# Performance work log

Measured on AMD Instinct MI355X. Metric: run time of the kernel, lower is better.

The kernel has to match this reference:

```python
import jax, jax.numpy as jnp
import numpy as np

N = 100000
NNZ = 1600000
C_IN = 128
C_OUT = 128


def setup_inputs() -> dict:
    key = jax.random.key(0)
    ks = jax.random.split(key, 9)
    phi_indices = jax.random.randint(ks[0], (2, NNZ), 0, N, dtype=jnp.int64)
    phi_values = jax.random.uniform(ks[1], (NNZ,), dtype=jnp.float32)
    phi_inverse_indices = jax.random.randint(ks[2], (2, NNZ), 0, N, dtype=jnp.int64)
    phi_inverse_values = jax.random.uniform(ks[3], (NNZ,), dtype=jnp.float32)
    # feature matrix is N x C_IN sparse: row in [0,N), col in [0,C_IN)
    f_rows = jax.random.randint(ks[4], (NNZ,), 0, N, dtype=jnp.int64)
    f_cols = jax.random.randint(ks[5], (NNZ,), 0, C_IN, dtype=jnp.int64)
    feature_indices = jnp.stack([f_rows, f_cols], axis=0)
    feature_values = jax.random.uniform(ks[6], (NNZ,), dtype=jnp.float32)
    # xavier-uniform weight, diagonal filter ~ U(0.9, 1.1)
    limit = float(np.sqrt(6.0 / (C_IN + C_OUT)))
    weight_matrix = jax.random.uniform(ks[7], (C_IN, C_OUT), minval=-limit, maxval=limit, dtype=jnp.float32)
    diagonal_weight_filter = jax.random.uniform(ks[8], (N, 1), minval=0.9, maxval=1.1, dtype=jnp.float32)
    return {
        "phi_indices": phi_indices,
        "phi_values": phi_values,
        "phi_inverse_indices": phi_inverse_indices,
        "phi_inverse_values": phi_inverse_values,
        "feature_indices": feature_indices,
        "feature_values": feature_values,
        "weight_matrix": weight_matrix,
        "diagonal_weight_filter": diagonal_weight_filter,
        "dropout": 0,
    }


def _spmm(indices, values, dense, n_rows):
    # sparse (n_rows x K) @ dense (K x C): gather dense rows by col index,
    # scale by values, scatter-add into output rows.
    rows, cols = indices[0], indices[1]
    contrib = values[:, None] * dense[cols]  # [nnz, C]
    return jax.ops.segment_sum(contrib, rows, num_segments=n_rows)


def reference(phi_indices, phi_values, phi_inverse_indices, phi_inverse_values,
              feature_indices, feature_values, weight_matrix,
              diagonal_weight_filter, dropout):
    n = diagonal_weight_filter.shape[0]
    # filtered = F_sparse @ W   -> [N, C_out]
    filtered = _spmm(feature_indices, feature_values, weight_matrix, n)
    # Phi @ diag(theta) @ Phi_inv @ filtered, computed right-to-left:
    z = _spmm(phi_inverse_indices, phi_inverse_values, filtered, n)  # Phi_inv @ filtered
    z = diagonal_weight_filter * z  # row-rescale by diagonal Theta
    localized = _spmm(phi_indices, phi_values, z, n)  # Phi @ (...)
    # F.dropout with training=False is identity; relu only
    return jax.nn.relu(localized)
```

## Files before the change

### kernel.cpp

```cpp
#include <hip/hip_runtime.h>

#define CH 128
#define SUMS_BLOCK 512
#define CHUNK_E 4096
#define RPT 16
#define BUCKET_BITS 10
#define BKEYS (1 << BUCKET_BITS)
#define NBMAX 512
#define STAG_CAP 18432

__device__ inline ushort f2bf(float f) {
    unsigned b = __float_as_uint(f);
    return (ushort)((b + 0x7FFF + ((b >> 16) & 1)) >> 16);
}
__device__ inline float bf2f(ushort u) {
    return __uint_as_float((unsigned)u << 16);
}

__global__ void conv_w_kernel(const float* __restrict__ W,
                              ushort* __restrict__ Wb) {
    int i = blockIdx.x * blockDim.x + threadIdx.x;
    if (i < CH * CH) Wb[i] = f2bf(W[i]);
}

__global__ __launch_bounds__(256) void passA_sort(const int* __restrict__ idxA,
                                                  const float* __restrict__ valA,
                                                  const int* __restrict__ idxB,
                                                  const float* __restrict__ valB,
                                                  const int* __restrict__ idxC,
                                                  const float* __restrict__ valC,
                                                  const float* __restrict__ theta,
                                                  int nnz, int n, int nb,
                                                  int* __restrict__ locA,
                                                  int2* __restrict__ recsTmp) {
    __shared__ int hist[NBMAX];
    __shared__ int sc[NBMAX];
    __shared__ int cur[NBMAX];
    int t = threadIdx.x;
    hist[t] = 0; hist[t + 256] = 0;
    __syncthreads();

    int base = blockIdx.x * CHUNK_E;
    int end = min(base + CHUNK_E, 3 * nnz);
    int csize = end - base;
    int rbeg = base + t * RPT;

    int px[RPT];
    int pv[RPT];
    short pb[RPT];

    int nvalid = 0;
    if (rbeg + RPT <= nnz) {
        #pragma unroll
        for (int r4 = 0; r4 < RPT / 4; ++r4) {
            int4 k4 = *reinterpret_cast<const int4*>(&idxA[rbeg + r4 * 4]);
            int4 c4 = *reinterpret_cast<const int4*>(&idxA[nnz + rbeg + r4 * 4]);
            float4 v4 = *reinterpret_cast<const float4*>(&valA[rbeg + r4 * 4]);
            int kk[4] = {k4.x, k4.y, k4.z, k4.w};
            int cc[4] = {c4.x, c4.y, c4.z, c4.w};
            float vv[4] = {v4.x, v4.y, v4.z, v4.w};
            #pragma unroll
            for (int u = 0; u < 4; ++u) {
                int r = r4 * 4 + u;
                px[r] = cc[u] | ((kk[u] & (BKEYS - 1)) << 17);
                pv[r] = __float_as_int(vv[u]);
                pb[r] = (short)(kk[u] >> BUCKET_BITS);
                atomicAdd(&hist[pb[r]], 1);
            }
        }
        nvalid = RPT;
    } else if (rbeg >= nnz && rbeg + RPT <= 2 * nnz) {
        int e0 = rbeg - nnz;
        #pragma unroll
        for (int r4 = 0; r4 < RPT / 4; ++r4) {
            int4 k4 = *reinterpret_cast<const int4*>(&idxB[e0 + r4 * 4]);
            int4 c4 = *reinterpret_cast<const int4*>(&idxB[nnz + e0 + r4 * 4]);
            float4 v4 = *reinterpret_cast<const float4*>(&valB[e0 + r4 * 4]);
            int kk[4] = {k4.x, k4.y, k4.z, k4.w};
            int cc[4] = {c4.x, c4.y, c4.z, c4.w};
            float vv[4] = {v4.x, v4.y, v4.z, v4.w};
            #pragma unroll
            for (int u = 0; u < 4; ++u) {
                int r = r4 * 4 + u;
                int key = n + kk[u];
                px[r] = cc[u] | ((key & (BKEYS - 1)) << 17);
                pv[r] = __float_as_int(vv[u] * theta[cc[u]]);
                pb[r] = (short)(key >> BUCKET_BITS);
                atomicAdd(&hist[pb[r]], 1);
            }
        }
        nvalid = RPT;
    } else if (rbeg >= 2 * nnz && rbeg + RPT <= 3 * nnz) {
        int e0 = rbeg - 2 * nnz;
        #pragma unroll
        for (int r4 = 0; r4 < RPT / 4; ++r4) {
            int4 k4 = *reinterpret_cast<const int4*>(&idxC[e0 + r4 * 4]);
            int4 c4 = *reinterpret_cast<const int4*>(&idxC[nnz + e0 + r4 * 4]);
            float4 v4 = *reinterpret_cast<const float4*>(&valC[e0 + r4 * 4]);
            int kk[4] = {k4.x, k4.y, k4.z, k4.w};
            int cc[4] = {c4.x, c4.y, c4.z, c4.w};
            float vv[4] = {v4.x, v4.y, v4.z, v4.w};
            #pragma unroll
            for (int u = 0; u < 4; ++u) {
                int r = r4 * 4 + u;
                int key = 2 * n + kk[u];
                px[r] = cc[u] | ((key & (BKEYS - 1)) << 17);
                pv[r] = __float_as_int(vv[u]);
                pb[r] = (short)(key >> BUCKET_BITS);
                atomicAdd(&hist[pb[r]], 1);
            }
        }
        nvalid = RPT;
    } else {
        #pragma unroll
        for (int r = 0; r < RPT; ++r) {
            int i = rbeg + r;
            if (i >= end) break;
            int key, c;
            float v;
            if (i < nnz) {
                key = idxA[i];
                c = idxA[nnz + i];
                v = valA[i];
            } else if (i < 2 * nnz) {
                int e = i - nnz;
                key = n + idxB[e];
                c = idxB[nnz + e];
                v = valB[e] * theta[c];
            } else {
                int e = i - 2 * nnz;
                key = 2 * n + idxC[e];
                c = idxC[nnz + e];
                v = valC[e];
            }
            px[r] = c | ((key & (BKEYS - 1)) << 17);
            pv[r] = __float_as_int(v);
            pb[r] = (short)(key >> BUCKET_BITS);
            atomicAdd(&hist[pb[r]], 1);
            ++nvalid;
        }
    }
    __syncthreads();

    sc[t] = hist[t]; sc[t + 256] = hist[t + 256];
    __syncthreads();
    for (int off = 1; off < NBMAX; off <<= 1) {
        int a = (t >= off) ? sc[t - off] : 0;
        int b2 = (t + 256 >= off) ? sc[t + 256 - off] : 0;
        __syncthreads();
        sc[t] += a; sc[t + 256] += b2;
        __syncthreads();
    }
    cur[t] = sc[t] - hist[t];
    cur[t + 256] = sc[t + 256] - hist[t + 256];
    __syncthreads();

    for (int b = t; b <= nb; b += 256)
        locA[(size_t)blockIdx.x * (nb + 1) + b] = (b < nb) ? (sc[b] - hist[b]) : csize;

    #pragma unroll
    for (int r = 0; r < RPT; ++r) {
        if (r < nvalid) {
            int pos = atomicAdd(&cur[pb[r]], 1);
            recsTmp[(size_t)base + pos] = make_int2(px[r], pv[r]);
        }
    }
}

__global__ __launch_bounds__(256) void bucket_totals(const int* __restrict__ locA,
                                                     int nchA, int nb,
                                                     int* __restrict__ tot) {
    __shared__ int red[256];
    int b = blockIdx.x;
    int t = threadIdx.x;
    int s = 0;
    for (int ch = t; ch < nchA; ch += 256) {
        const int* lc = &locA[(size_t)ch * (nb + 1)];
        s += lc[b + 1] - lc[b];
    }
    red[t] = s;
    __syncthreads();
    for (int off = 128; off > 0; off >>= 1) {
        if (t < off) red[t] += red[t + off];
        __syncthreads();
    }
    if (t == 0) tot[b] = red[0];
}

__global__ void scan_sums_kernel(int* __restrict__ chunk_sums, int nchunks) {
    __shared__ int tmp[SUMS_BLOCK];
    __shared__ int carry_s;
    int tid = threadIdx.x;
    if (tid == 0) carry_s = 0;
    __syncthreads();
    for (int base = 0; base < nchunks; base += SUMS_BLOCK) {
        int i = base + tid;
        int v = (i < nchunks) ? chunk_sums[i] : 0;
        tmp[tid] = v;
        __syncthreads();
        for (int off = 1; off < SUMS_BLOCK; off <<= 1) {
            int y = (tid >= off) ? tmp[tid - off] : 0;
            __syncthreads();
            tmp[tid] += y;
            __syncthreads();
        }
        int c = carry_s;
        if (i < nchunks) chunk_sums[i] = tmp[tid] - v + c;
        int total = tmp[SUMS_BLOCK - 1];
        __syncthreads();
        if (tid == 0) carry_s = c + total;
        __syncthreads();
    }
}

__global__ __launch_bounds__(1024) void passB_kernel(const int2* __restrict__ recsTmp,
                                                     const int* __restrict__ locA,
                                                     const int* __restrict__ bsArr,
                                                     int nchA, int nb, int n3,
                                                     int* __restrict__ start_g,
                                                     int* __restrict__ counts_g,
                                                     unsigned* __restrict__ recs) {
    __shared__ int hist[BKEYS];
    __shared__ int scan[BKEYS];
    __shared__ unsigned outb[STAG_CAP];
    int b = blockIdx.x;
    int t = threadIdx.x;
    int wave = t >> 6, lane = t & 63;
    int grp = lane >> 4, gl = lane & 15;
    int bs = bsArr[b];
    hist[t] = 0;
    __syncthreads();

    for (int ch = wave * 4 + grp; ch < nchA; ch += 64) {
        const int* lc = &locA[(size_t)ch * (nb + 1)];
        int ls = lc[b], le = lc[b + 1];
        size_t cb = (size_t)ch * CHUNK_E;
        for (int k = ls + gl; k < le; k += 16)
            atomicAdd(&hist[(recsTmp[cb + k].x >> 17) & (BKEYS - 1)], 1);
    }
    __syncthreads();

    int v = hist[t];
    scan[t] = v;
    __syncthreads();
    for (int off = 1; off < BKEYS; off <<= 1) {
        int y = (t >= off) ? scan[t - off] : 0;
        __syncthreads();
        scan[t] += y;
        __syncthreads();
    }
    int excl = scan[t] - v;
    int key = (b << BUCKET_BITS) + t;
    if (key < n3) {
        start_g[key] = bs + excl;
        counts_g[key] = v;
    }
    int totalB = scan[BKEYS - 1];
    hist[t] = excl;
    __syncthreads();

    if (totalB <= STAG_CAP) {
        for (int ch = wave * 4 + grp; ch < nchA; ch += 64) {
            const int* lc = &locA[(size_t)ch * (nb + 1)];
            int ls = lc[b], le = lc[b + 1];
            size_t cb = (size_t)ch * CHUNK_E;
            for (int k = ls + gl; k < le; k += 16) {
                int2 r = recsTmp[cb + k];
                int kk = (r.x >> 17) & (BKEYS - 1);
                int pos = atomicAdd(&hist[kk], 1);
                unsigned c = (unsigned)(r.x & 0x1FFFF);
                unsigned bv = (unsigned)f2bf(__int_as_float(r.y)) & 0x7FFFu;
                outb[pos] = (c << 15) | bv;
            }
        }
        __syncthreads();
        for (int k = t; k < totalB; k += 1024)
            recs[(size_t)bs + k] = outb[k];
    } else {
        for (int ch = wave * 4 + grp; ch < nchA; ch += 64) {
            const int* lc = &locA[(size_t)ch * (nb + 1)];
            int ls = lc[b], le = lc[b + 1];
            size_t cb = (size_t)ch * CHUNK_E;
            for (int k = ls + gl; k < le; k += 16) {
                int2 r = recsTmp[cb + k];
                int kk = (r.x >> 17) & (BKEYS - 1);
                int pos = atomicAdd(&hist[kk], 1);
                unsigned c = (unsigned)(r.x & 0x1FFFF);
                unsigned bv = (unsigned)f2bf(__int_as_float(r.y)) & 0x7FFFu;
                recs[(size_t)bs + pos] = (c << 15) | bv;
            }
        }
    }
}

__global__ __launch_bounds__(256) void pull_spmm_bf16(
        const unsigned* __restrict__ recs,
        const int* __restrict__ start,
        const int* __restrict__ counts,
        const ushort* __restrict__ dense,
        ushort* __restrict__ outb,
        float* __restrict__ outf,
        int n, int do_relu) {
    int grp32 = threadIdx.x >> 5;
    int lane = threadIdx.x & 31;
    int row = blockIdx.x * 8 + grp32;
    if (row >= n) return;
    int s = start[row];
    int cnt = counts[row];
    const ushort4* dp = reinterpret_cast<const ushort4*>(dense);
    float a0 = 0.0f, a1 = 0.0f, a2 = 0.0f, a3 = 0.0f;

    for (int jb = 0; jb < cnt; jb += 32) {
        int nbatch = min(32, cnt - jb);
        unsigned myrec = (lane < nbatch) ? recs[s + jb + lane] : 0u;
        int j = 0;
        for (; j + 4 <= nbatch; j += 4) {
            unsigned r0 = __shfl(myrec, j + 0, 32);
            unsigned r1 = __shfl(myrec, j + 1, 32);
            unsigned r2 = __shfl(myrec, j + 2, 32);
            unsigned r3 = __shfl(myrec, j + 3, 32);
            ushort4 d0 = dp[(size_t)(r0 >> 15) * 32 + lane];
            ushort4 d1 = dp[(size_t)(r1 >> 15) * 32 + lane];
            ushort4 d2 = dp[(size_t)(r2 >> 15) * 32 + lane];
            ushort4 d3 = dp[(size_t)(r3 >> 15) * 32 + lane];
            float v0 = __uint_as_float((r0 & 0x7FFFu) << 16);
            float v1 = __uint_as_float((r1 & 0x7FFFu) << 16);
            float v2 = __uint_as_float((r2 & 0x7FFFu) << 16);
            float v3 = __uint_as_float((r3 & 0x7FFFu) << 16);
            a0 = fmaf(v0, bf2f(d0.x), a0); a1 = fmaf(v0, bf2f(d0.y), a1);
            a2 = fmaf(v0, bf2f(d0.z), a2); a3 = fmaf(v0, bf2f(d0.w), a3);
            a0 = fmaf(v1, bf2f(d1.x), a0); a1 = fmaf(v1, bf2f(d1.y), a1);
            a2 = fmaf(v1, bf2f(d1.z), a2); a3 = fmaf(v1, bf2f(d1.w), a3);
            a0 = fmaf(v2, bf2f(d2.x), a0); a1 = fmaf(v2, bf2f(d2.y), a1);
            a2 = fmaf(v2, bf2f(d2.z), a2); a3 = fmaf(v2, bf2f(d2.w), a3);
            a0 = fmaf(v3, bf2f(d3.x), a0); a1 = fmaf(v3, bf2f(d3.y), a1);
            a2 = fmaf(v3, bf2f(d3.z), a2); a3 = fmaf(v3, bf2f(d3.w), a3);
        }
        for (; j < nbatch; ++j) {
            unsigned r0 = __shfl(myrec, j, 32);
            ushort4 d0 = dp[(size_t)(r0 >> 15) * 32 + lane];
            float v0 = __uint_as_float((r0 & 0x7FFFu) << 16);
            a0 = fmaf(v0, bf2f(d0.x), a0); a1 = fmaf(v0, bf2f(d0.y), a1);
            a2 = fmaf(v0, bf2f(d0.z), a2); a3 = fmaf(v0, bf2f(d0.w), a3);
        }
    }
    if (do_relu) {
        a0 = fmaxf(a0, 0.0f); a1 = fmaxf(a1, 0.0f);
        a2 = fmaxf(a2, 0.0f); a3 = fmaxf(a3, 0.0f);
    }
    if (outb) {
        ushort4 o = {f2bf(a0), f2bf(a1), f2bf(a2), f2bf(a3)};
        reinterpret_cast<ushort4*>(outb)[(size_t)row * 32 + lane] = o;
    } else {
        float4 o = {a0, a1, a2, a3};
        *reinterpret_cast<float4*>(&outf[(size_t)row * CH + lane * 4]) = o;
    }
}


extern "C" void kernel_launch(void* const* d_in, const int* in_sizes, int n_in,
                              void* d_out, int out_size, void* d_ws, size_t ws_size,
                              hipStream_t stream) {
    const int*   phi_idx  = (const int*)d_in[0];
    const float* phi_val  = (const float*)d_in[1];
    const int*   phii_idx = (const int*)d_in[2];
    const float* phii_val = (const float*)d_in[3];
    const int*   f_idx    = (const int*)d_in[4];
    const float* f_val    = (const float*)d_in[5];
    const float* W        = (const float*)d_in[6];
    const float* theta    = (const float*)d_in[7];

    const int nnz = in_sizes[1];
    const int n   = in_sizes[7];
    const int n3  = 3 * n;
    const int total = 3 * nnz;

    const int nb   = (n3 + BKEYS - 1) >> BUCKET_BITS;
    const int nchA = (total + CHUNK_E - 1) / CHUNK_E;

    float* out = (float*)d_out;

    char* ws = (char*)d_ws;
    char*  dense_region = ws;
    int2*  recsTmp  = (int2*)dense_region;
    ushort* filt_b  = (ushort*)dense_region;
    ushort* z_b     = (ushort*)(dense_region + (size_t)n * CH * sizeof(ushort));
    ws += (size_t)n * CH * sizeof(float);
    unsigned* recs  = (unsigned*)ws;        ws += (size_t)total * sizeof(unsigned);
    int* counts     = (int*)ws;             ws += (size_t)n3 * sizeof(int);
    int* start      = (int*)ws;             ws += (size_t)n3 * sizeof(int);
    int* locA       = (int*)ws;             ws += (size_t)nchA * (nb + 1) * sizeof(int);
    int* tot        = (int*)ws;             ws += 4096;
    ushort* w_b     = (ushort*)ws;          ws += CH * CH * sizeof(ushort);

    const int row_blocks = (n + 7) / 8;

    conv_w_kernel<<<(CH * CH + 255) / 256, 256, 0, stream>>>(W, w_b);

    passA_sort<<<nchA, 256, 0, stream>>>(phii_idx, phii_val, phi_idx, phi_val,
                                         f_idx, f_val, theta,
                                         nnz, n, nb, locA, recsTmp);
    bucket_totals<<<nb, 256, 0, stream>>>(locA, nchA, nb, tot);
    scan_sums_kernel<<<1, SUMS_BLOCK, 0, stream>>>(tot, nb);
    passB_kernel<<<nb, 1024, 0, stream>>>(recsTmp, locA, tot, nchA, nb, n3,
                                          start, counts, recs);

    pull_spmm_bf16<<<row_blocks, 256, 0, stream>>>(
        recs, start + 2 * n, counts + 2 * n, w_b, filt_b, nullptr, n, 0);

    pull_spmm_bf16<<<row_blocks, 256, 0, stream>>>(
        recs, start, counts, filt_b, z_b, nullptr, n, 0);

    pull_spmm_bf16<<<row_blocks, 256, 0, stream>>>(
        recs, start + n, counts + n, z_b, nullptr, out, n, 1);
}
```

Measured before the change: 236.6 us.

## Pack sort records early and widen SpMM loads to 16-byte bf16 vectors

The first sort pass now converts each value to bf16 and packs it with the column into a 4-byte record. The in-bucket key goes into a separate 2-byte array, replacing the 8-byte int2 temporary, so the second pass reads less data and just copies the packed record. The pull SpMM kernel now uses 16 lanes per row, each loading a uint4 (8 bf16 values), instead of 32 lanes loading ushort4, which halves the number of gather instructions per nonzero. The trade-off is more accumulator registers per thread and a narrower shuffle width.

After: 250.4 us. 1.06x slower.

```diff
diff --git a/kernel.cpp b/kernel.cpp
--- a/kernel.cpp
+++ b/kernel.cpp
@@ -12,9 +12,6 @@
 __device__ inline ushort f2bf(float f) {
     unsigned b = __float_as_uint(f);
     return (ushort)((b + 0x7FFF + ((b >> 16) & 1)) >> 16);
-}
-__device__ inline float bf2f(ushort u) {
-    return __uint_as_float((unsigned)u << 16);
 }
 
 __global__ void conv_w_kernel(const float* __restrict__ W,
@@ -32,7 +29,8 @@
                                                   const float* __restrict__ theta,
                                                   int nnz, int n, int nb,
                                                   int* __restrict__ locA,
-                                                  int2* __restrict__ recsTmp) {
+                                                  unsigned* __restrict__ recs4Tmp,
+                                                  ushort* __restrict__ keyTmp) {
     __shared__ int hist[NBMAX];
     __shared__ int sc[NBMAX];
     __shared__ int cur[NBMAX];
@@ -45,8 +43,8 @@
     int csize = end - base;
     int rbeg = base + t * RPT;
 
-    int px[RPT];
-    int pv[RPT];
+    unsigned px[RPT];
+    ushort pk[RPT];
     short pb[RPT];
 
     int nvalid = 0;
@@ -62,8 +60,8 @@
             #pragma unroll
             for (int u = 0; u < 4; ++u) {
                 int r = r4 * 4 + u;
-                px[r] = cc[u] | ((kk[u] & (BKEYS - 1)) << 17);
-                pv[r] = __float_as_int(vv[u]);
+                px[r] = ((unsigned)cc[u] << 15) | ((unsigned)f2bf(vv[u]) & 0x7FFFu);
+                pk[r] = (ushort)(kk[u] & (BKEYS - 1));
                 pb[r] = (short)(kk[u] >> BUCKET_BITS);
                 atomicAdd(&hist[pb[r]], 1);
             }
@@ -83,8 +81,9 @@
             for (int u = 0; u < 4; ++u) {
                 int r = r4 * 4 + u;
                 int key = n + kk[u];
-                px[r] = cc[u] | ((key & (BKEYS - 1)) << 17);
-                pv[r] = __float_as_int(vv[u] * theta[cc[u]]);
+                px[r] = ((unsigned)cc[u] << 15) |
+                        ((unsigned)f2bf(vv[u] * theta[cc[u]]) & 0x7FFFu);
+                pk[r] = (ushort)(key & (BKEYS - 1));
                 pb[r] = (short)(key >> BUCKET_BITS);
                 atomicAdd(&hist[pb[r]], 1);
             }
@@ -104,8 +103,8 @@
             for (int u = 0; u < 4; ++u) {
                 int r = r4 * 4 + u;
                 int key = 2 * n + kk[u];
-                px[r] = cc[u] | ((key & (BKEYS - 1)) << 17);
-                pv[r] = __float_as_int(vv[u]);
+                px[r] = ((unsigned)cc[u] << 15) | ((unsigned)f2bf(vv[u]) & 0x7FFFu);
+                pk[r] = (ushort)(key & (BKEYS - 1));
                 pb[r] = (short)(key >> BUCKET_BITS);
                 atomicAdd(&hist[pb[r]], 1);
             }
@@ -133,8 +132,8 @@
                 c = idxC[nnz + e];
                 v = valC[e];
             }
-            px[r] = c | ((key & (BKEYS - 1)) << 17);
-            pv[r] = __float_as_int(v);
+            px[r] = ((unsigned)c << 15) | ((unsigned)f2bf(v) & 0x7FFFu);
+            pk[r] = (ushort)(key & (BKEYS - 1));
             pb[r] = (short)(key >> BUCKET_BITS);
             atomicAdd(&hist[pb[r]], 1);
             ++nvalid;
@@ -162,7 +161,8 @@
     for (int r = 0; r < RPT; ++r) {
         if (r < nvalid) {
             int pos = atomicAdd(&cur[pb[r]], 1);
-            recsTmp[(size_t)base + pos] = make_int2(px[r], pv[r]);
+            recs4Tmp[(size_t)base + pos] = px[r];
+            keyTmp[(size_t)base + pos] = pk[r];
         }
     }
 }
@@ -213,7 +213,8 @@
     }
 }
 
-__global__ __launch_bounds__(1024) void passB_kernel(const int2* __restrict__ recsTmp,
+__global__ __launch_bounds__(1024) void passB_kernel(const unsigned* __restrict__ recs4Tmp,
+                                                     const ushort* __restrict__ keyTmp,
                                                      const int* __restrict__ locA,
                                                      const int* __restrict__ bsArr,
                                                      int nchA, int nb, int n3,
@@ -236,7 +237,7 @@
         int ls = lc[b], le = lc[b + 1];
         size_t cb = (size_t)ch * CHUNK_E;
         for (int k = ls + gl; k < le; k += 16)
-            atomicAdd(&hist[(recsTmp[cb + k].x >> 17) & (BKEYS - 1)], 1);
+            atomicAdd(&hist[keyTmp[cb + k]], 1);
     }
     __syncthreads();
 
@@ -265,12 +266,9 @@
             int ls = lc[b], le = lc[b + 1];
             size_t cb = (size_t)ch * CHUNK_E;
             for (int k = ls + gl; k < le; k += 16) {
-                int2 r = recsTmp[cb + k];
-                int kk = (r.x >> 17) & (BKEYS - 1);
+                int kk = keyTmp[cb + k];
                 int pos = atomicAdd(&hist[kk], 1);
-                unsigned c = (unsigned)(r.x & 0x1FFFF);
-                unsigned bv = (unsigned)f2bf(__int_as_float(r.y)) & 0x7FFFu;
-                outb[pos] = (c << 15) | bv;
+                outb[pos] = recs4Tmp[cb + k];
             }
         }
         __syncthreads();
@@ -282,12 +280,9 @@
             int ls = lc[b], le = lc[b + 1];
             size_t cb = (size_t)ch * CHUNK_E;
             for (int k = ls + gl; k < le; k += 16) {
-                int2 r = recsTmp[cb + k];
-                int kk = (r.x >> 17) & (BKEYS - 1);
+                int kk = keyTmp[cb + k];
                 int pos = atomicAdd(&hist[kk], 1);
-                unsigned c = (unsigned)(r.x & 0x1FFFF);
-                unsigned bv = (unsigned)f2bf(__int_as_float(r.y)) & 0x7FFFu;
-                recs[(size_t)bs + pos] = (c << 15) | bv;
+                recs[(size_t)bs + pos] = recs4Tmp[cb + k];
             }
         }
     }
@@ -301,59 +296,71 @@
         ushort* __restrict__ outb,
         float* __restrict__ outf,
         int n, int do_relu) {
-    int grp32 = threadIdx.x >> 5;
-    int lane = threadIdx.x & 31;
-    int row = blockIdx.x * 8 + grp32;
+    int grp = threadIdx.x >> 4;
+    int lane = threadIdx.x & 15;
+    int row = blockIdx.x * 16 + grp;
     if (row >= n) return;
     int s = start[row];
     int cnt = counts[row];
-    const ushort4* dp = reinterpret_cast<const ushort4*>(dense);
-    float a0 = 0.0f, a1 = 0.0f, a2 = 0.0f, a3 = 0.0f;
-
-    for (int jb = 0; jb < cnt; jb += 32) {
-        int nbatch = min(32, cnt - jb);
+    const uint4* dp = reinterpret_cast<const uint4*>(dense);
+    float a0 = 0, a1 = 0, a2 = 0, a3 = 0, a4 = 0, a5 = 0, a6 = 0, a7 = 0;
+
+    #define ACC(dv, vf) \
+        a0 = fmaf(vf, __uint_as_float((dv).x << 16), a0);           \
+        a1 = fmaf(vf, __uint_as_float((dv).x & 0xFFFF0000u), a1);   \
+        a2 = fmaf(vf, __uint_as_float((dv).y << 16), a2);           \
+        a3 = fmaf(vf, __uint_as_float((dv).y & 0xFFFF0000u), a3);   \
+        a4 = fmaf(vf, __uint_as_float((dv).z << 16), a4);           \
+        a5 = fmaf(vf, __uint_as_float((dv).z & 0xFFFF0000u), a5);   \
+        a6 = fmaf(vf, __uint_as_float((dv).w << 16), a6);           \
+        a7 = fmaf(vf, __uint_as_float((dv).w & 0xFFFF0000u), a7);
+
+    for (int jb = 0; jb < cnt; jb += 16) {
+        int nbatch = min(16, cnt - jb);
         unsigned myrec = (lane < nbatch) ? recs[s + jb + lane] : 0u;
         int j = 0;
         for (; j + 4 <= nbatch; j += 4) {
-            unsigned r0 = __shfl(myrec, j + 0, 32);
-            unsigned r1 = __shfl(myrec, j + 1, 32);
-            unsigned r2 = __shfl(myrec, j + 2, 32);
-            unsigned r3 = __shfl(myrec, j + 3, 32);
-            ushort4 d0 = dp[(size_t)(r0 >> 15) * 32 + lane];
-            ushort4 d1 = dp[(size_t)(r1 >> 15) * 32 + lane];
-            ushort4 d2 = dp[(size_t)(r2 >> 15) * 32 + lane];
-            ushort4 d3 = dp[(size_t)(r3 >> 15) * 32 + lane];
+            unsigned r0 = __shfl(myrec, j + 0, 16);
+            unsigned r1 = __shfl(myrec, j + 1, 16);
+            unsigned r2 = __shfl(myrec, j + 2, 16);
+            unsigned r3 = __shfl(myrec, j + 3, 16);
+            uint4 d0 = dp[(size_t)(r0 >> 15) * 16 + lane];
+            uint4 d1 = dp[(size_t)(r1 >> 15) * 16 + lane];
+            uint4 d2 = dp[(size_t)(r2 >> 15) * 16 + lane];
+            uint4 d3 = dp[(size_t)(r3 >> 15) * 16 + lane];
             float v0 = __uint_as_float((r0 & 0x7FFFu) << 16);
             float v1 = __uint_as_float((r1 & 0x7FFFu) << 16);
             float v2 = __uint_as_float((r2 & 0x7FFFu) << 16);
             float v3 = __uint_as_float((r3 & 0x7FFFu) << 16);
-            a0 = fmaf(v0, bf2f(d0.x), a0); a1 = fmaf(v0, bf2f(d0.y), a1);
-            a2 = fmaf(v0, bf2f(d0.z), a2); a3 = fmaf(v0, bf2f(d0.w), a3);
-            a0 = fmaf(v1, bf2f(d1.x), a0); a1 = fmaf(v1, bf2f(d1.y), a1);
-            a2 = fmaf(v1, bf2f(d1.z), a2); a3 = fmaf(v1, bf2f(d1.w), a3);
-            a0 = fmaf(v2, bf2f(d2.x), a0); a1 = fmaf(v2, bf2f(d2.y), a1);
-            a2 = fmaf(v2, bf2f(d2.z), a2); a3 = fmaf(v2, bf2f(d2.w), a3);
-            a0 = fmaf(v3, bf2f(d3.x), a0); a1 = fmaf(v3, bf2f(d3.y), a1);
-            a2 = fmaf(v3, bf2f(d3.z), a2); a3 = fmaf(v3, bf2f(d3.w), a3);
+            ACC(d0, v0) ACC(d1, v1) ACC(d2, v2) ACC(d3, v3)
         }
         for (; j < nbatch; ++j) {
-            unsigned r0 = __shfl(myrec, j, 32);
-            ushort4 d0 = dp[(size_t)(r0 >> 15) * 32 + lane];
+            unsigned r0 = __shfl(myrec, j, 16);
+            uint4 d0 = dp[(size_t)(r0 >> 15) * 16 + lane];
             float v0 = __uint_as_float((r0 & 0x7FFFu) << 16);
-            a0 = fmaf(v0, bf2f(d0.x), a0); a1 = fmaf(v0, bf2f(d0.y), a1);
-            a2 = fmaf(v0, bf2f(d0.z), a2); a3 = fmaf(v0, bf2f(d0.w), a3);
-        }
-    }
+            ACC(d0, v0)
+        }
+    }
+    #undef ACC
+
     if (do_relu) {
         a0 = fmaxf(a0, 0.0f); a1 = fmaxf(a1, 0.0f);
         a2 = fmaxf(a2, 0.0f); a3 = fmaxf(a3, 0.0f);
+        a4 = fmaxf(a4, 0.0f); a5 = fmaxf(a5, 0.0f);
+        a6 = fmaxf(a6, 0.0f); a7 = fmaxf(a7, 0.0f);
     }
     if (outb) {
-        ushort4 o = {f2bf(a0), f2bf(a1), f2bf(a2), f2bf(a3)};
-        reinterpret_cast<ushort4*>(outb)[(size_t)row * 32 + lane] = o;
+        uint4 o;
+        o.x = (unsigned)f2bf(a0) | ((unsigned)f2bf(a1) << 16);
+        o.y = (unsigned)f2bf(a2) | ((unsigned)f2bf(a3) << 16);
+        o.z = (unsigned)f2bf(a4) | ((unsigned)f2bf(a5) << 16);
+        o.w = (unsigned)f2bf(a6) | ((unsigned)f2bf(a7) << 16);
+        reinterpret_cast<uint4*>(outb)[(size_t)row * 16 + lane] = o;
     } else {
-        float4 o = {a0, a1, a2, a3};
-        *reinterpret_cast<float4*>(&outf[(size_t)row * CH + lane * 4]) = o;
+        float4 o0 = {a0, a1, a2, a3};
+        float4 o1 = {a4, a5, a6, a7};
+        *reinterpret_cast<float4*>(&outf[(size_t)row * CH + lane * 8]) = o0;
+        *reinterpret_cast<float4*>(&outf[(size_t)row * CH + lane * 8 + 4]) = o1;
     }
 }
 
@@ -382,7 +389,8 @@
 
     char* ws = (char*)d_ws;
     char*  dense_region = ws;
-    int2*  recsTmp  = (int2*)dense_region;
+    unsigned* recs4Tmp = (unsigned*)dense_region;
+    ushort* keyTmp  = (ushort*)(dense_region + (size_t)total * sizeof(unsigned));
     ushort* filt_b  = (ushort*)dense_region;
     ushort* z_b     = (ushort*)(dense_region + (size_t)n * CH * sizeof(ushort));
     ws += (size_t)n * CH * sizeof(float);
@@ -393,16 +401,16 @@
     int* tot        = (int*)ws;             ws += 4096;
     ushort* w_b     = (ushort*)ws;          ws += CH * CH * sizeof(ushort);
 
-    const int row_blocks = (n + 7) / 8;
+    const int row_blocks = (n + 15) / 16;
 
     conv_w_kernel<<<(CH * CH + 255) / 256, 256, 0, stream>>>(W, w_b);
 
     passA_sort<<<nchA, 256, 0, stream>>>(phii_idx, phii_val, phi_idx, phi_val,
                                          f_idx, f_val, theta,
-                                         nnz, n, nb, locA, recsTmp);
+                                         nnz, n, nb, locA, recs4Tmp, keyTmp);
     bucket_totals<<<nb, 256, 0, stream>>>(locA, nchA, nb, tot);
     scan_sums_kernel<<<1, SUMS_BLOCK, 0, stream>>>(tot, nb);
-    passB_kernel<<<nb, 1024, 0, stream>>>(recsTmp, locA, tot, nchA, nb, n3,
+    passB_kernel<<<nb, 1024, 0, stream>>>(recs4Tmp, keyTmp, locA, tot, nchA, nb, n3,
                                           start, counts, recs);
 
     pull_spmm_bf16<<<row_blocks, 256, 0, stream>>>(
```

## Fuse feature-times-weight SpMM into bucket-sort pass B using LDS-resident weights

Applied to the files above, without the earlier changes.

The first SpMM (sparse features times W) now runs inside passB_kernel for the buckets holding feature-matrix keys. Those blocks load the bf16 weight matrix into shared memory and accumulate each row straight from the staged records. This removes one kernel launch and the global write and re-read of those records. The cost is 32KB more LDS per block, which may reduce occupancy of the sort pass. The workspace is also rearranged so filt_b no longer aliases recsTmp.

Result: slower. 298.8 us (+26.3%).

```diff
diff --git a/kernel.cpp b/kernel.cpp
--- a/kernel.cpp
+++ b/kernel.cpp
@@ -216,19 +216,27 @@
 __global__ __launch_bounds__(1024) void passB_kernel(const int2* __restrict__ recsTmp,
                                                      const int* __restrict__ locA,
                                                      const int* __restrict__ bsArr,
-                                                     int nchA, int nb, int n3,
+                                                     const uint4* __restrict__ w4,
+                                                     ushort* __restrict__ filt_b,
+                                                     int nchA, int nb, int n, int n3,
                                                      int* __restrict__ start_g,
                                                      int* __restrict__ counts_g,
                                                      unsigned* __restrict__ recs) {
     __shared__ int hist[BKEYS];
     __shared__ int scan[BKEYS];
     __shared__ unsigned outb[STAG_CAP];
+    __shared__ uint4 Wlds[CH * 16];
     int b = blockIdx.x;
     int t = threadIdx.x;
     int wave = t >> 6, lane = t & 63;
     int grp = lane >> 4, gl = lane & 15;
     int bs = bsArr[b];
+    int keyBase = b << BUCKET_BITS;
+    int k2 = 2 * n - keyBase;
+    bool hasF = (k2 < BKEYS);
     hist[t] = 0;
+    if (hasF)
+        for (int i = t; i < CH * 16; i += 1024) Wlds[i] = w4[i];
     __syncthreads();
 
     for (int ch = wave * 4 + grp; ch < nchA; ch += 64) {
@@ -250,7 +258,7 @@
         __syncthreads();
     }
     int excl = scan[t] - v;
-    int key = (b << BUCKET_BITS) + t;
+    int key = keyBase + t;
     if (key < n3) {
         start_g[key] = bs + excl;
         counts_g[key] = v;
@@ -258,6 +266,21 @@
     int totalB = scan[BKEYS - 1];
     hist[t] = excl;
     __syncthreads();
+
+    int flushEnd;
+    if (k2 >= BKEYS)      flushEnd = totalB;
+    else if (k2 <= 0)     flushEnd = 0;
+    else                  flushEnd = scan[k2 - 1];
+
+    #define FACC(wv, vf) \
+        a0 = fmaf(vf, __uint_as_float((wv).x << 16), a0);           \
+        a1 = fmaf(vf, __uint_as_float((wv).x & 0xFFFF0000u), a1);   \
+        a2 = fmaf(vf, __uint_as_float((wv).y << 16), a2);           \
+        a3 = fmaf(vf, __uint_as_float((wv).y & 0xFFFF0000u), a3);   \
+        a4 = fmaf(vf, __uint_as_float((wv).z << 16), a4);           \
+        a5 = fmaf(vf, __uint_as_float((wv).z & 0xFFFF0000u), a5);   \
+        a6 = fmaf(vf, __uint_as_float((wv).w << 16), a6);           \
+        a7 = fmaf(vf, __uint_as_float((wv).w & 0xFFFF0000u), a7);
 
     if (totalB <= STAG_CAP) {
         for (int ch = wave * 4 + grp; ch < nchA; ch += 64) {
@@ -274,8 +297,30 @@
             }
         }
         __syncthreads();
-        for (int k = t; k < totalB; k += 1024)
+        for (int k = t; k < flushEnd; k += 1024)
             recs[(size_t)bs + k] = outb[k];
+        if (hasF) {
+            int grp64 = t >> 4, l16 = t & 15;
+            for (int idx = grp64; idx < BKEYS; idx += 64) {
+                int ky = keyBase + idx;
+                if (ky < 2 * n || ky >= n3) continue;
+                int rs = idx ? scan[idx - 1] : 0;
+                int re = scan[idx];
+                float a0 = 0, a1 = 0, a2 = 0, a3 = 0, a4 = 0, a5 = 0, a6 = 0, a7 = 0;
+                for (int j = rs; j < re; ++j) {
+                    unsigned rec = outb[j];
+                    float vf = __uint_as_float((rec & 0x7FFFu) << 16);
+                    uint4 wv = Wlds[(rec >> 15) * 16 + l16];
+                    FACC(wv, vf)
+                }
+                uint4 o;
+                o.x = (unsigned)f2bf(a0) | ((unsigned)f2bf(a1) << 16);
+                o.y = (unsigned)f2bf(a2) | ((unsigned)f2bf(a3) << 16);
+                o.z = (unsigned)f2bf(a4) | ((unsigned)f2bf(a5) << 16);
+                o.w = (unsigned)f2bf(a6) | ((unsigned)f2bf(a7) << 16);
+                reinterpret_cast<uint4*>(filt_b)[(size_t)(ky - 2 * n) * 16 + l16] = o;
+            }
+        }
     } else {
         for (int ch = wave * 4 + grp; ch < nchA; ch += 64) {
             const int* lc = &locA[(size_t)ch * (nb + 1)];
@@ -290,7 +335,31 @@
                 recs[(size_t)bs + pos] = (c << 15) | bv;
             }
         }
-    }
+        __syncthreads();
+        if (hasF) {
+            int grp64 = t >> 4, l16 = t & 15;
+            for (int idx = grp64; idx < BKEYS; idx += 64) {
+                int ky = keyBase + idx;
+                if (ky < 2 * n || ky >= n3) continue;
+                int rs = idx ? scan[idx - 1] : 0;
+                int re = scan[idx];
+                float a0 = 0, a1 = 0, a2 = 0, a3 = 0, a4 = 0, a5 = 0, a6 = 0, a7 = 0;
+                for (int j = rs; j < re; ++j) {
+                    unsigned rec = recs[(size_t)bs + j];
+                    float vf = __uint_as_float((rec & 0x7FFFu) << 16);
+                    uint4 wv = Wlds[(rec >> 15) * 16 + l16];
+                    FACC(wv, vf)
+                }
+                uint4 o;
+                o.x = (unsigned)f2bf(a0) | ((unsigned)f2bf(a1) << 16);
+                o.y = (unsigned)f2bf(a2) | ((unsigned)f2bf(a3) << 16);
+                o.z = (unsigned)f2bf(a4) | ((unsigned)f2bf(a5) << 16);
+                o.w = (unsigned)f2bf(a6) | ((unsigned)f2bf(a7) << 16);
+                reinterpret_cast<uint4*>(filt_b)[(size_t)(ky - 2 * n) * 16 + l16] = o;
+            }
+        }
+    }
+    #undef FACC
 }
 
 __global__ __launch_bounds__(256) void pull_spmm_bf16(
@@ -381,17 +450,17 @@
     float* out = (float*)d_out;
 
     char* ws = (char*)d_ws;
-    char*  dense_region = ws;
-    int2*  recsTmp  = (int2*)dense_region;
-    ushort* filt_b  = (ushort*)dense_region;
-    ushort* z_b     = (ushort*)(dense_region + (size_t)n * CH * sizeof(ushort));
-    ws += (size_t)n * CH * sizeof(float);
+    char* region0   = ws;
+    int2* recsTmp   = (int2*)region0;
+    ushort* z_b     = (ushort*)region0;
+    ws += (size_t)total * sizeof(int2);
     unsigned* recs  = (unsigned*)ws;        ws += (size_t)total * sizeof(unsigned);
     int* counts     = (int*)ws;             ws += (size_t)n3 * sizeof(int);
     int* start      = (int*)ws;             ws += (size_t)n3 * sizeof(int);
     int* locA       = (int*)ws;             ws += (size_t)nchA * (nb + 1) * sizeof(int);
     int* tot        = (int*)ws;             ws += 4096;
     ushort* w_b     = (ushort*)ws;          ws += CH * CH * sizeof(ushort);
+    ushort* filt_b  = (ushort*)ws;          ws += (size_t)n * CH * sizeof(ushort);
 
     const int row_blocks = (n + 7) / 8;
 
@@ -402,11 +471,10 @@
                                          nnz, n, nb, locA, recsTmp);
     bucket_totals<<<nb, 256, 0, stream>>>(locA, nchA, nb, tot);
     scan_sums_kernel<<<1, SUMS_BLOCK, 0, stream>>>(tot, nb);
-    passB_kernel<<<nb, 1024, 0, stream>>>(recsTmp, locA, tot, nchA, nb, n3,
+    passB_kernel<<<nb, 1024, 0, stream>>>(recsTmp, locA, tot,
+                                          (const uint4*)w_b, filt_b,
+                                          nchA, nb, n, n3,
                                           start, counts, recs);
-
-    pull_spmm_bf16<<<row_blocks, 256, 0, stream>>>(
-        recs, start + 2 * n, counts + 2 * n, w_b, filt_b, nullptr, n, 0);
 
     pull_spmm_bf16<<<row_blocks, 256, 0, stream>>>(
         recs, start, counts, filt_b, z_b, nullptr, n, 0);
```
